# Optimization experiments

Measured on AMD Instinct MI355X. Metric: run time of the kernel, lower is better.

The kernel has to match this reference:

```python
import jax, jax.numpy as jnp
import numpy as np

DIM = 384
NUM_HEADS = 12
DILATIONS = (1, 2, 3)
KSZ = 3
B, N = 4, 8192
HEAD_DIM = DIM // NUM_HEADS          # 32
ND = len(DILATIONS)                  # num_dilation
CD = DIM // ND                       # channels per dilation group
SCALE = HEAD_DIM ** -0.5


def setup_inputs() -> dict:
    key = jax.random.key(0)
    k0, k1, k2 = jax.random.split(key, 3)
    s = 0.02
    return {
        "x": jax.random.normal(k0, (B, N, DIM), dtype=jnp.float32),
        "Wqkv": jax.random.normal(k1, (3 * DIM, DIM), dtype=jnp.float32) * s,
        "bqkv": jnp.zeros((3 * DIM,), dtype=jnp.float32),
        "Wproj": jax.random.normal(k2, (DIM, DIM), dtype=jnp.float32) * s,
        "bproj": jnp.zeros((DIM,), dtype=jnp.float32),
    }


def _unfold_seq(t, dil, ksz):
    # Faithful nn.Unfold(ksz, dilation=dil, padding=dil*(ksz-1)//2) applied to
    # t viewed as (B, C, N, 1): of the ksz*ksz taps, only the center-width
    # column is in-bounds; the rest are zero padding. Tap order is (kh, kw)
    # with kw fastest, matching torch's unfold channel layout.
    # t: (B, nh, hd, N) -> (B, nh, hd, ksz*ksz, N)
    _, _, _, n = t.shape
    pad = dil * (ksz - 1) // 2
    tp = jnp.pad(t, ((0, 0), (0, 0), (0, 0), (pad, pad)))
    zeros = jnp.zeros_like(t)
    taps = []
    for kh in range(ksz):
        row = jax.lax.dynamic_slice_in_dim(tp, kh * dil, n, axis=3)
        for kw in range(ksz):
            taps.append(row if kw == ksz // 2 else zeros)
    return jnp.stack(taps, axis=3)


def _dilate_attn(q, k, v, dil):
    # q,k,v: (B, CD, N) -> (B, N, CD)
    b, cd, n = q.shape
    nh = cd // HEAD_DIM
    q = q.reshape(b, nh, HEAD_DIM, n)
    k = _unfold_seq(k.reshape(b, nh, HEAD_DIM, n), dil, KSZ)   # (b,nh,hd,k2,n)
    v = _unfold_seq(v.reshape(b, nh, HEAD_DIM, n), dil, KSZ)
    attn = jax.nn.softmax(jnp.einsum("bhdn,bhdjn->bhnj", q, k) * SCALE, axis=-1)
    out = jnp.einsum("bhnj,bhdjn->bhnd", attn, v)              # (b,nh,n,hd)
    return out.transpose(0, 2, 1, 3).reshape(b, n, cd)


def reference(x, Wqkv, bqkv, Wproj, bproj):
    b, n, c = x.shape
    # (b,n,3c) -> (nd, 3, b, cd, n), matching torch permute(3,2,0,4,1)
    qkv = (x @ Wqkv.T + bqkv).reshape(b, n, 3, ND, CD).transpose(3, 2, 0, 4, 1)
    outs = [_dilate_attn(qkv[i, 0], qkv[i, 1], qkv[i, 2], DILATIONS[i]) for i in range(ND)]
    xo = jnp.stack(outs, axis=2).reshape(b, n, c)  # (b,n,nd,cd) -> (b,n,c)
    return xo @ Wproj.T + bproj
```

## Files before the change

### kernel.cpp

```cpp
#include <hip/hip_runtime.h>

#define DIM     384
#define QKV_CH  1152
#define HD      32
#define CD      128
#define BATCH   4
#define SEQ     8192
#define ROWS    (BATCH*SEQ)
#define SCALE   0.17677669529663687f

#define KB8         48
#define FRAG_STRIDE (KB8*128)
#define XRB_MAX     (ROWS/16 - 1)
#define LSTR        136

typedef short bf16x8 __attribute__((ext_vector_type(8)));
typedef float f32x4  __attribute__((ext_vector_type(4)));

__device__ __forceinline__ unsigned short f2bf(float f) {
  unsigned int u = __float_as_uint(f);
  u += 0x7fffu + ((u >> 16) & 1u);
  return (unsigned short)(u >> 16);
}
__device__ __forceinline__ float bf2f(unsigned short b) {
  return __uint_as_float(((unsigned int)b) << 16);
}
__device__ __forceinline__ void unpack4(uint2 u, float* f) {
  f[0] = bf2f((unsigned short)(u.x & 0xffffu)); f[1] = bf2f((unsigned short)(u.x >> 16));
  f[2] = bf2f((unsigned short)(u.y & 0xffffu)); f[3] = bf2f((unsigned short)(u.y >> 16));
}


template<int K>
__global__ __launch_bounds__(256) void cvt_swz(const float* __restrict__ in,
                                               unsigned short* __restrict__ out) {
  const int KB = K / 8;
  int cid = blockIdx.x * 256 + threadIdx.x;
  int rl = cid & 15;
  int q  = cid >> 4;
  int rb = q / KB;
  int kb = q - rb * KB;
  const float* p = in + (size_t)(rb * 16 + rl) * K + kb * 8;
  float4 a = *(const float4*)p;
  float4 b = *(const float4*)(p + 4);
  unsigned int w0 = (unsigned int)f2bf(a.x) | ((unsigned int)f2bf(a.y) << 16);
  unsigned int w1 = (unsigned int)f2bf(a.z) | ((unsigned int)f2bf(a.w) << 16);
  unsigned int w2 = (unsigned int)f2bf(b.x) | ((unsigned int)f2bf(b.y) << 16);
  unsigned int w3 = (unsigned int)f2bf(b.z) | ((unsigned int)f2bf(b.w) << 16);
  uint4 u; u.x = w0; u.y = w1; u.z = w2; u.w = w3;
  *(uint4*)(out + (size_t)cid * 8) = u;
}

template<int OUT_BF16, int K, int NT>
__global__ __launch_bounds__(256) void gemm_swz(const unsigned short* __restrict__ A,
                                                const unsigned short* __restrict__ Bt,
                                                const float* __restrict__ bias,
                                                void* __restrict__ Cv) {
  const int KB = K / 8;
  const int t = threadIdx.x;
  const int wave = t >> 6, lane = t & 63;
  const int quad = lane >> 4, l16 = lane & 15;
  const int row0 = blockIdx.x * 128, col0 = blockIdx.y * 128;
  const int wm = (wave & 1) * 64, wn = (wave >> 1) * 64;

  const unsigned short* PA[4];
  const unsigned short* PB[4];
#pragma unroll
  for (int mi = 0; mi < 4; ++mi)
    PA[mi] = A + (size_t)(((row0 + wm) >> 4) + mi) * KB * 128 + lane * 8;
#pragma unroll
  for (int ni = 0; ni < 4; ++ni)
    PB[ni] = Bt + (size_t)(((col0 + wn) >> 4) + ni) * KB * 128 + lane * 8;

  f32x4 acc[4][4] = {};

#pragma unroll
  for (int kk = 0; kk < K / 32; ++kk) {
    bf16x8 af[4], bfv[4];
#pragma unroll
    for (int mi = 0; mi < 4; ++mi) af[mi]  = *(const bf16x8*)(PA[mi] + kk * 512);
#pragma unroll
    for (int ni = 0; ni < 4; ++ni) bfv[ni] = *(const bf16x8*)(PB[ni] + kk * 512);
#pragma unroll
    for (int mi = 0; mi < 4; ++mi)
#pragma unroll
      for (int ni = 0; ni < 4; ++ni)
        acc[mi][ni] = __builtin_amdgcn_mfma_f32_16x16x32_bf16(bfv[ni], af[mi], acc[mi][ni], 0, 0, 0);
  }

  float4 bv[4];
#pragma unroll
  for (int ni = 0; ni < 4; ++ni)
    bv[ni] = *(const float4*)&bias[col0 + wn + ni * 16 + quad * 4];

#pragma unroll
  for (int mi = 0; mi < 4; ++mi) {
    size_t gr = (size_t)(row0 + wm + mi * 16 + l16);
#pragma unroll
    for (int ni = 0; ni < 4; ++ni) {
      int gc = col0 + wn + ni * 16 + quad * 4;
      float v0 = acc[mi][ni][0] + bv[ni].x;
      float v1 = acc[mi][ni][1] + bv[ni].y;
      float v2 = acc[mi][ni][2] + bv[ni].z;
      float v3 = acc[mi][ni][3] + bv[ni].w;
      if (OUT_BF16) {
        uint2 u;
        u.x = (unsigned int)f2bf(v0) | ((unsigned int)f2bf(v1) << 16);
        u.y = (unsigned int)f2bf(v2) | ((unsigned int)f2bf(v3) << 16);
        *(uint2*)&((unsigned short*)Cv)[gr * NT + gc] = u;
      } else {
        float4 o; o.x = v0; o.y = v1; o.z = v2; o.w = v3;
        *(float4*)&((float*)Cv)[gr * NT + gc] = o;
      }
    }
  }
}

__global__ __launch_bounds__(256, 2) void fused_qkv_attn(
    const unsigned short* __restrict__ X,
    const unsigned short* __restrict__ W,
    const float* __restrict__ bqkv,
    unsigned short* __restrict__ out) {
  __shared__ unsigned short sm[34816];
  unsigned short* q_t = sm;
  unsigned short* k_t = sm + 64 * LSTR;
  unsigned short* v_t = sm + 160 * LSTR;

  const int t = threadIdx.x;
  const int w = t >> 6, lane = t & 63;
  const int quad = lane >> 4, l16 = lane & 15;
  const int d = blockIdx.y;
  const int row0 = blockIdx.x * 64;
  const int rb0 = row0 >> 4;

  const unsigned short* pa[6];
#pragma unroll
  for (int j = 0; j < 6; ++j) {
    int xrb = rb0 - 1 + j;
    xrb = xrb < 0 ? 0 : (xrb > XRB_MAX ? XRB_MAX : xrb);
    pa[j] = X + (size_t)xrb * FRAG_STRIDE + lane * 8;
  }
  const unsigned short *pbq[2], *pbk[2], *pbv[2];
#pragma unroll
  for (int c = 0; c < 2; ++c) {
    int wrb = d * 8 + w * 2 + c;
    pbq[c] = W + (size_t)wrb * FRAG_STRIDE + lane * 8;
    pbk[c] = W + (size_t)(wrb + 24) * FRAG_STRIDE + lane * 8;
    pbv[c] = W + (size_t)(wrb + 48) * FRAG_STRIDE + lane * 8;
  }

  f32x4 aq[4][2] = {}, ak[6][2] = {}, av[6][2] = {};

#pragma unroll
  for (int kk = 0; kk < 12; ++kk) {
    bf16x8 a[6];
#pragma unroll
    for (int j = 0; j < 6; ++j) a[j] = *(const bf16x8*)(pa[j] + kk * 512);
    bf16x8 bq[2], bk[2], bv[2];
#pragma unroll
    for (int c = 0; c < 2; ++c) {
      bq[c] = *(const bf16x8*)(pbq[c] + kk * 512);
      bk[c] = *(const bf16x8*)(pbk[c] + kk * 512);
      bv[c] = *(const bf16x8*)(pbv[c] + kk * 512);
    }
#pragma unroll
    for (int c = 0; c < 2; ++c) {
#pragma unroll
      for (int j = 0; j < 4; ++j)
        aq[j][c] = __builtin_amdgcn_mfma_f32_16x16x32_bf16(bq[c], a[j + 1], aq[j][c], 0, 0, 0);
#pragma unroll
      for (int j = 0; j < 6; ++j)
        ak[j][c] = __builtin_amdgcn_mfma_f32_16x16x32_bf16(bk[c], a[j], ak[j][c], 0, 0, 0);
#pragma unroll
      for (int j = 0; j < 6; ++j)
        av[j][c] = __builtin_amdgcn_mfma_f32_16x16x32_bf16(bv[c], a[j], av[j][c], 0, 0, 0);
    }
  }

#pragma unroll
  for (int c = 0; c < 2; ++c) {
    int colb = w * 32 + c * 16 + quad * 4;
    float4 b_q = *(const float4*)&bqkv[d * CD + colb];
    float4 b_k = *(const float4*)&bqkv[384 + d * CD + colb];
    float4 b_v = *(const float4*)&bqkv[768 + d * CD + colb];
#pragma unroll
    for (int j = 0; j < 4; ++j) {
      uint2 u;
      u.x = (unsigned int)f2bf(aq[j][c][0] + b_q.x) | ((unsigned int)f2bf(aq[j][c][1] + b_q.y) << 16);
      u.y = (unsigned int)f2bf(aq[j][c][2] + b_q.z) | ((unsigned int)f2bf(aq[j][c][3] + b_q.w) << 16);
      *(uint2*)&q_t[(j * 16 + l16) * LSTR + colb] = u;
    }
#pragma unroll
    for (int j = 0; j < 6; ++j) {
      uint2 u;
      u.x = (unsigned int)f2bf(ak[j][c][0] + b_k.x) | ((unsigned int)f2bf(ak[j][c][1] + b_k.y) << 16);
      u.y = (unsigned int)f2bf(ak[j][c][2] + b_k.z) | ((unsigned int)f2bf(ak[j][c][3] + b_k.w) << 16);
      *(uint2*)&k_t[(j * 16 + l16) * LSTR + colb] = u;
    }
#pragma unroll
    for (int j = 0; j < 6; ++j) {
      uint2 u;
      u.x = (unsigned int)f2bf(av[j][c][0] + b_v.x) | ((unsigned int)f2bf(av[j][c][1] + b_v.y) << 16);
      u.y = (unsigned int)f2bf(av[j][c][2] + b_v.z) | ((unsigned int)f2bf(av[j][c][3] + b_v.w) << 16);
      *(uint2*)&v_t[(j * 16 + l16) * LSTR + colb] = u;
    }
  }
  __syncthreads();

  const int h = t >> 6;
  const int r = t & 63;
  const int dil = d + 1;
  const int n = (row0 + r) & (SEQ - 1);

  float q[32];
  {
    const uint2* qp = (const uint2*)&q_t[r * LSTR + h * HD];
#pragma unroll
    for (int c = 0; c < 8; ++c) unpack4(qp[c], &q[c * 4]);
  }

  float ex[3];
  int   valid[3];
#pragma unroll
  for (int kh = 0; kh < 3; ++kh) {
    int off = (kh - 1) * dil;
    int nn = n + off;
    int v = (nn >= 0) && (nn < SEQ);
    valid[kh] = v;
    float l = 0.f;
    if (v) {
      const uint2* kp = (const uint2*)&k_t[(r + 16 + off) * LSTR + h * HD];
#pragma unroll
      for (int c = 0; c < 8; ++c) {
        float kkv[4]; unpack4(kp[c], kkv);
#pragma unroll
        for (int j = 0; j < 4; ++j) l += q[c * 4 + j] * kkv[j];
      }
    }
    ex[kh] = v ? __expf(l * SCALE) : 1.f;
  }
  float inv = 1.f / (ex[0] + ex[1] + ex[2] + 6.f);

  float o[32];
#pragma unroll
  for (int e = 0; e < 32; ++e) o[e] = 0.f;
#pragma unroll
  for (int kh = 0; kh < 3; ++kh) {
    if (!valid[kh]) continue;
    int off = (kh - 1) * dil;
    const uint2* vp = (const uint2*)&v_t[(r + 16 + off) * LSTR + h * HD];
    float wgt = ex[kh];
#pragma unroll
    for (int c = 0; c < 8; ++c) {
      float vv[4]; unpack4(vp[c], vv);
#pragma unroll
      for (int j = 0; j < 4; ++j) o[c * 4 + j] += wgt * vv[j];
    }
  }

  int row = row0 + r;
  int ch0 = d * CD + h * HD;
  unsigned short* op = out + ((size_t)(row >> 4) * KB8 + (ch0 >> 3)) * 128 + (row & 15) * 8;
#pragma unroll
  for (int c = 0; c < 4; ++c) {
    uint4 u;
    u.x = (unsigned int)f2bf(o[c*8+0] * inv) | ((unsigned int)f2bf(o[c*8+1] * inv) << 16);
    u.y = (unsigned int)f2bf(o[c*8+2] * inv) | ((unsigned int)f2bf(o[c*8+3] * inv) << 16);
    u.z = (unsigned int)f2bf(o[c*8+4] * inv) | ((unsigned int)f2bf(o[c*8+5] * inv) << 16);
    u.w = (unsigned int)f2bf(o[c*8+6] * inv) | ((unsigned int)f2bf(o[c*8+7] * inv) << 16);
    *(uint4*)(op + c * 128) = u;
  }
}

extern "C" void kernel_launch(void* const* d_in, const int* in_sizes, int n_in,
                              void* d_out, int out_size, void* d_ws, size_t ws_size,
                              hipStream_t stream) {
  const float* x     = (const float*)d_in[0];
  const float* Wqkv  = (const float*)d_in[1];
  const float* bqkv  = (const float*)d_in[2];
  const float* Wproj = (const float*)d_in[3];
  const float* bproj = (const float*)d_in[4];
  float* out = (float*)d_out;

  char* ws = (char*)d_ws;
  unsigned short* x_swz     = (unsigned short*)(ws);
  unsigned short* attn_swz  = (unsigned short*)(ws + 25165824);
  unsigned short* wqkv_swz  = (unsigned short*)(ws + 50331648);
  unsigned short* wproj_swz = (unsigned short*)(ws + 51216384);

  cvt_swz<DIM><<<ROWS * (DIM / 8) / 256, 256, 0, stream>>>(x, x_swz);
  cvt_swz<DIM><<<QKV_CH * (DIM / 8) / 256, 256, 0, stream>>>(Wqkv, wqkv_swz);
  cvt_swz<DIM><<<DIM * (DIM / 8) / 256, 256, 0, stream>>>(Wproj, wproj_swz);

  fused_qkv_attn<<<dim3(ROWS / 64, 3), 256, 0, stream>>>(x_swz, wqkv_swz, bqkv, attn_swz);

  gemm_swz<0, DIM, DIM><<<dim3(ROWS / 128, DIM / 128), 256, 0, stream>>>(
      attn_swz, wproj_swz, bproj, (void*)out);
}
```

Baseline: 169.8 us.

## Widen fused QKV-attention block to 512 threads with swizzled LDS and merged conversion

The three fp32-to-bf16 swizzle conversions are merged into one launch. The fused QKV+attention kernel moves from 256 to 512 threads per block. Each wave now computes one 16-column slice instead of two, and each attention thread handles half a head with a shuffle reduction for the dot product. Padded LDS rows are replaced with an XOR swizzle to cut shared-memory use and avoid bank conflicts. The aim is to lower per-thread registers and raise occupancy and parallelism, at the cost of each wave re-reading the X fragments and an extra cross-lane shuffle.

```diff
diff --git a/kernel.cpp b/kernel.cpp
--- a/kernel.cpp
+++ b/kernel.cpp
@@ -12,7 +12,6 @@
 #define KB8         48
 #define FRAG_STRIDE (KB8*128)
 #define XRB_MAX     (ROWS/16 - 1)
-#define LSTR        136
 
 typedef short bf16x8 __attribute__((ext_vector_type(8)));
 typedef float f32x4  __attribute__((ext_vector_type(4)));
@@ -30,24 +29,34 @@
   f[2] = bf2f((unsigned short)(u.y & 0xffffu)); f[3] = bf2f((unsigned short)(u.y >> 16));
 }
 
-
-template<int K>
-__global__ __launch_bounds__(256) void cvt_swz(const float* __restrict__ in,
-                                               unsigned short* __restrict__ out) {
-  const int KB = K / 8;
+__device__ __forceinline__ int swz(int row, int col) {
+  return (row * 128 + col) ^ ((row & 31) << 2);
+}
+
+
+__global__ __launch_bounds__(256) void cvt_all(const float* __restrict__ x,
+                                               const float* __restrict__ wqkv,
+                                               const float* __restrict__ wproj,
+                                               unsigned short* __restrict__ xo,
+                                               unsigned short* __restrict__ qo,
+                                               unsigned short* __restrict__ po) {
   int cid = blockIdx.x * 256 + threadIdx.x;
+  const float* in; unsigned short* out;
+  if (cid < 1572864) { in = x; out = xo; }
+  else if (cid < 1628160) { cid -= 1572864; in = wqkv; out = qo; }
+  else { cid -= 1628160; in = wproj; out = po; }
   int rl = cid & 15;
   int q  = cid >> 4;
-  int rb = q / KB;
-  int kb = q - rb * KB;
-  const float* p = in + (size_t)(rb * 16 + rl) * K + kb * 8;
+  int rb = q / KB8;
+  int kb = q - rb * KB8;
+  const float* p = in + (size_t)(rb * 16 + rl) * DIM + kb * 8;
   float4 a = *(const float4*)p;
   float4 b = *(const float4*)(p + 4);
-  unsigned int w0 = (unsigned int)f2bf(a.x) | ((unsigned int)f2bf(a.y) << 16);
-  unsigned int w1 = (unsigned int)f2bf(a.z) | ((unsigned int)f2bf(a.w) << 16);
-  unsigned int w2 = (unsigned int)f2bf(b.x) | ((unsigned int)f2bf(b.y) << 16);
-  unsigned int w3 = (unsigned int)f2bf(b.z) | ((unsigned int)f2bf(b.w) << 16);
-  uint4 u; u.x = w0; u.y = w1; u.z = w2; u.w = w3;
+  uint4 u;
+  u.x = (unsigned int)f2bf(a.x) | ((unsigned int)f2bf(a.y) << 16);
+  u.y = (unsigned int)f2bf(a.z) | ((unsigned int)f2bf(a.w) << 16);
+  u.z = (unsigned int)f2bf(b.x) | ((unsigned int)f2bf(b.y) << 16);
+  u.w = (unsigned int)f2bf(b.z) | ((unsigned int)f2bf(b.w) << 16);
   *(uint4*)(out + (size_t)cid * 8) = u;
 }
 
@@ -116,15 +125,15 @@
   }
 }
 
-__global__ __launch_bounds__(256, 2) void fused_qkv_attn(
+__global__ __launch_bounds__(512, 4) void fused_qkv_attn(
     const unsigned short* __restrict__ X,
     const unsigned short* __restrict__ W,
     const float* __restrict__ bqkv,
     unsigned short* __restrict__ out) {
-  __shared__ unsigned short sm[34816];
+  __shared__ unsigned short sm[32768];
   unsigned short* q_t = sm;
-  unsigned short* k_t = sm + 64 * LSTR;
-  unsigned short* v_t = sm + 160 * LSTR;
+  unsigned short* k_t = sm + 64 * 128;
+  unsigned short* v_t = sm + 160 * 128;
 
   const int t = threadIdx.x;
   const int w = t >> 6, lane = t & 63;
@@ -140,83 +149,73 @@
     xrb = xrb < 0 ? 0 : (xrb > XRB_MAX ? XRB_MAX : xrb);
     pa[j] = X + (size_t)xrb * FRAG_STRIDE + lane * 8;
   }
-  const unsigned short *pbq[2], *pbk[2], *pbv[2];
-#pragma unroll
-  for (int c = 0; c < 2; ++c) {
-    int wrb = d * 8 + w * 2 + c;
-    pbq[c] = W + (size_t)wrb * FRAG_STRIDE + lane * 8;
-    pbk[c] = W + (size_t)(wrb + 24) * FRAG_STRIDE + lane * 8;
-    pbv[c] = W + (size_t)(wrb + 48) * FRAG_STRIDE + lane * 8;
-  }
-
-  f32x4 aq[4][2] = {}, ak[6][2] = {}, av[6][2] = {};
+  const int wrb = d * 8 + w;
+  const unsigned short* pbq = W + (size_t)wrb * FRAG_STRIDE + lane * 8;
+  const unsigned short* pbk = pbq + (size_t)24 * FRAG_STRIDE;
+  const unsigned short* pbv = pbq + (size_t)48 * FRAG_STRIDE;
+
+  f32x4 aq[4] = {}, ak[6] = {}, av[6] = {};
 
 #pragma unroll
   for (int kk = 0; kk < 12; ++kk) {
     bf16x8 a[6];
 #pragma unroll
     for (int j = 0; j < 6; ++j) a[j] = *(const bf16x8*)(pa[j] + kk * 512);
-    bf16x8 bq[2], bk[2], bv[2];
-#pragma unroll
-    for (int c = 0; c < 2; ++c) {
-      bq[c] = *(const bf16x8*)(pbq[c] + kk * 512);
-      bk[c] = *(const bf16x8*)(pbk[c] + kk * 512);
-      bv[c] = *(const bf16x8*)(pbv[c] + kk * 512);
-    }
-#pragma unroll
-    for (int c = 0; c < 2; ++c) {
-#pragma unroll
-      for (int j = 0; j < 4; ++j)
-        aq[j][c] = __builtin_amdgcn_mfma_f32_16x16x32_bf16(bq[c], a[j + 1], aq[j][c], 0, 0, 0);
-#pragma unroll
-      for (int j = 0; j < 6; ++j)
-        ak[j][c] = __builtin_amdgcn_mfma_f32_16x16x32_bf16(bk[c], a[j], ak[j][c], 0, 0, 0);
-#pragma unroll
-      for (int j = 0; j < 6; ++j)
-        av[j][c] = __builtin_amdgcn_mfma_f32_16x16x32_bf16(bv[c], a[j], av[j][c], 0, 0, 0);
-    }
-  }
-
-#pragma unroll
-  for (int c = 0; c < 2; ++c) {
-    int colb = w * 32 + c * 16 + quad * 4;
+    bf16x8 bq = *(const bf16x8*)(pbq + kk * 512);
+    bf16x8 bk = *(const bf16x8*)(pbk + kk * 512);
+    bf16x8 bv = *(const bf16x8*)(pbv + kk * 512);
+#pragma unroll
+    for (int j = 0; j < 4; ++j)
+      aq[j] = __builtin_amdgcn_mfma_f32_16x16x32_bf16(bq, a[j + 1], aq[j], 0, 0, 0);
+#pragma unroll
+    for (int j = 0; j < 6; ++j)
+      ak[j] = __builtin_amdgcn_mfma_f32_16x16x32_bf16(bk, a[j], ak[j], 0, 0, 0);
+#pragma unroll
+    for (int j = 0; j < 6; ++j)
+      av[j] = __builtin_amdgcn_mfma_f32_16x16x32_bf16(bv, a[j], av[j], 0, 0, 0);
+  }
+
+  const int colb = w * 16 + quad * 4;
+  {
     float4 b_q = *(const float4*)&bqkv[d * CD + colb];
     float4 b_k = *(const float4*)&bqkv[384 + d * CD + colb];
     float4 b_v = *(const float4*)&bqkv[768 + d * CD + colb];
 #pragma unroll
     for (int j = 0; j < 4; ++j) {
       uint2 u;
-      u.x = (unsigned int)f2bf(aq[j][c][0] + b_q.x) | ((unsigned int)f2bf(aq[j][c][1] + b_q.y) << 16);
-      u.y = (unsigned int)f2bf(aq[j][c][2] + b_q.z) | ((unsigned int)f2bf(aq[j][c][3] + b_q.w) << 16);
-      *(uint2*)&q_t[(j * 16 + l16) * LSTR + colb] = u;
+      u.x = (unsigned int)f2bf(aq[j][0] + b_q.x) | ((unsigned int)f2bf(aq[j][1] + b_q.y) << 16);
+      u.y = (unsigned int)f2bf(aq[j][2] + b_q.z) | ((unsigned int)f2bf(aq[j][3] + b_q.w) << 16);
+      *(uint2*)&q_t[swz(j * 16 + l16, colb)] = u;
     }
 #pragma unroll
     for (int j = 0; j < 6; ++j) {
       uint2 u;
-      u.x = (unsigned int)f2bf(ak[j][c][0] + b_k.x) | ((unsigned int)f2bf(ak[j][c][1] + b_k.y) << 16);
-      u.y = (unsigned int)f2bf(ak[j][c][2] + b_k.z) | ((unsigned int)f2bf(ak[j][c][3] + b_k.w) << 16);
-      *(uint2*)&k_t[(j * 16 + l16) * LSTR + colb] = u;
+      u.x = (unsigned int)f2bf(ak[j][0] + b_k.x) | ((unsigned int)f2bf(ak[j][1] + b_k.y) << 16);
+      u.y = (unsigned int)f2bf(ak[j][2] + b_k.z) | ((unsigned int)f2bf(ak[j][3] + b_k.w) << 16);
+      *(uint2*)&k_t[swz(j * 16 + l16, colb)] = u;
     }
 #pragma unroll
     for (int j = 0; j < 6; ++j) {
       uint2 u;
-      u.x = (unsigned int)f2bf(av[j][c][0] + b_v.x) | ((unsigned int)f2bf(av[j][c][1] + b_v.y) << 16);
-      u.y = (unsigned int)f2bf(av[j][c][2] + b_v.z) | ((unsigned int)f2bf(av[j][c][3] + b_v.w) << 16);
-      *(uint2*)&v_t[(j * 16 + l16) * LSTR + colb] = u;
+      u.x = (unsigned int)f2bf(av[j][0] + b_v.x) | ((unsigned int)f2bf(av[j][1] + b_v.y) << 16);
+      u.y = (unsigned int)f2bf(av[j][2] + b_v.z) | ((unsigned int)f2bf(av[j][3] + b_v.w) << 16);
+      *(uint2*)&v_t[swz(j * 16 + l16, colb)] = u;
     }
   }
   __syncthreads();
 
-  const int h = t >> 6;
-  const int r = t & 63;
+  const int p  = t & 1;
+  const int r  = (t >> 1) & 63;
+  const int h  = t >> 7;
   const int dil = d + 1;
   const int n = (row0 + r) & (SEQ - 1);
-
-  float q[32];
-  {
-    const uint2* qp = (const uint2*)&q_t[r * LSTR + h * HD];
-#pragma unroll
-    for (int c = 0; c < 8; ++c) unpack4(qp[c], &q[c * 4]);
+  const int c0 = h * HD + p * 16;
+
+  float q[16];
+#pragma unroll
+  for (int c = 0; c < 4; ++c) {
+    uint2 u = *(const uint2*)&q_t[swz(r, c0 + c * 4)];
+    unpack4(u, &q[c * 4]);
   }
 
   float ex[3];
@@ -227,42 +226,41 @@
     int nn = n + off;
     int v = (nn >= 0) && (nn < SEQ);
     valid[kh] = v;
-    float l = 0.f;
+    float partial = 0.f;
     if (v) {
-      const uint2* kp = (const uint2*)&k_t[(r + 16 + off) * LSTR + h * HD];
-#pragma unroll
-      for (int c = 0; c < 8; ++c) {
-        float kkv[4]; unpack4(kp[c], kkv);
-#pragma unroll
-        for (int j = 0; j < 4; ++j) l += q[c * 4 + j] * kkv[j];
+#pragma unroll
+      for (int c = 0; c < 4; ++c) {
+        uint2 u = *(const uint2*)&k_t[swz(r + 16 + off, c0 + c * 4)];
+        float kv[4]; unpack4(u, kv);
+#pragma unroll
+        for (int j = 0; j < 4; ++j) partial += q[c * 4 + j] * kv[j];
       }
     }
-    ex[kh] = v ? __expf(l * SCALE) : 1.f;
+    float full = partial + __shfl_xor(partial, 1);
+    ex[kh] = v ? __expf(full * SCALE) : 1.f;
   }
   float inv = 1.f / (ex[0] + ex[1] + ex[2] + 6.f);
 
-  float o[32];
-#pragma unroll
-  for (int e = 0; e < 32; ++e) o[e] = 0.f;
+  float o[16] = {};
 #pragma unroll
   for (int kh = 0; kh < 3; ++kh) {
     if (!valid[kh]) continue;
     int off = (kh - 1) * dil;
-    const uint2* vp = (const uint2*)&v_t[(r + 16 + off) * LSTR + h * HD];
     float wgt = ex[kh];
 #pragma unroll
-    for (int c = 0; c < 8; ++c) {
-      float vv[4]; unpack4(vp[c], vv);
+    for (int c = 0; c < 4; ++c) {
+      uint2 u = *(const uint2*)&v_t[swz(r + 16 + off, c0 + c * 4)];
+      float vv[4]; unpack4(u, vv);
 #pragma unroll
       for (int j = 0; j < 4; ++j) o[c * 4 + j] += wgt * vv[j];
     }
   }
 
   int row = row0 + r;
-  int ch0 = d * CD + h * HD;
+  int ch0 = d * CD + c0;
   unsigned short* op = out + ((size_t)(row >> 4) * KB8 + (ch0 >> 3)) * 128 + (row & 15) * 8;
 #pragma unroll
-  for (int c = 0; c < 4; ++c) {
+  for (int c = 0; c < 2; ++c) {
     uint4 u;
     u.x = (unsigned int)f2bf(o[c*8+0] * inv) | ((unsigned int)f2bf(o[c*8+1] * inv) << 16);
     u.y = (unsigned int)f2bf(o[c*8+2] * inv) | ((unsigned int)f2bf(o[c*8+3] * inv) << 16);
@@ -288,11 +286,9 @@
   unsigned short* wqkv_swz  = (unsigned short*)(ws + 50331648);
   unsigned short* wproj_swz = (unsigned short*)(ws + 51216384);
 
-  cvt_swz<DIM><<<ROWS * (DIM / 8) / 256, 256, 0, stream>>>(x, x_swz);
-  cvt_swz<DIM><<<QKV_CH * (DIM / 8) / 256, 256, 0, stream>>>(Wqkv, wqkv_swz);
-  cvt_swz<DIM><<<DIM * (DIM / 8) / 256, 256, 0, stream>>>(Wproj, wproj_swz);
-
-  fused_qkv_attn<<<dim3(ROWS / 64, 3), 256, 0, stream>>>(x_swz, wqkv_swz, bqkv, attn_swz);
+  cvt_all<<<6432, 256, 0, stream>>>(x, Wqkv, Wproj, x_swz, wqkv_swz, wproj_swz);
+
+  fused_qkv_attn<<<dim3(ROWS / 64, 3), 512, 0, stream>>>(x_swz, wqkv_swz, bqkv, attn_swz);
 
   gemm_swz<0, DIM, DIM><<<dim3(ROWS / 128, DIM / 128), 256, 0, stream>>>(
       attn_swz, wproj_swz, bproj, (void*)out);
```

After: 231.4 us. +36.3%, slower.
